# Optimization experiments

Hardware: AMD Instinct MI355X
Metric: run time of the kernel (lower is better)

## Reference

```python
import jax, jax.numpy as jnp
import numpy as np

B, S, I, H = 8, 2048, 8, 256
HEADS, HD = 4, 64
DECAY = 0.95


def _lstm_layer(x, w_ih, w_hh, b_ih, b_hh):
    # x: [B, S, in]; torch gate order i, f, g, o
    Hs = w_hh.shape[1]
    x_proj = jnp.einsum('bsi,gi->bsg', x, w_ih) + b_ih + b_hh  # [B,S,4H]
    def step(carry, xt):
        h, c = carry
        gates = xt + h @ w_hh.T
        i, f, g, o = jnp.split(gates, 4, axis=-1)
        c = jax.nn.sigmoid(f) * c + jax.nn.sigmoid(i) * jnp.tanh(g)
        h = jax.nn.sigmoid(o) * jnp.tanh(c)
        return (h, c), h
    h0 = jnp.zeros((x.shape[0], Hs), x.dtype)
    (_, _), hs = jax.lax.scan(step, (h0, h0), jnp.swapaxes(x_proj, 0, 1))
    return jnp.swapaxes(hs, 0, 1)  # [B,S,H]


def setup_inputs() -> dict:
    key = jax.random.key(0)
    ks = jax.random.split(key, 25)
    sc = lambda n: 1.0 / np.sqrt(n)
    d = {}
    d['x'] = jax.random.normal(ks[0], (B, S, I), jnp.float32)
    # LSTM layer 0 (in=I) and layer 1 (in=H)
    d['w_ih0'] = jax.random.uniform(ks[1], (4 * H, I), jnp.float32, -sc(H), sc(H))
    d['w_hh0'] = jax.random.uniform(ks[2], (4 * H, H), jnp.float32, -sc(H), sc(H))
    d['b_ih0'] = jax.random.uniform(ks[3], (4 * H,), jnp.float32, -sc(H), sc(H))
    d['b_hh0'] = jax.random.uniform(ks[4], (4 * H,), jnp.float32, -sc(H), sc(H))
    d['w_ih1'] = jax.random.uniform(ks[5], (4 * H, H), jnp.float32, -sc(H), sc(H))
    d['w_hh1'] = jax.random.uniform(ks[6], (4 * H, H), jnp.float32, -sc(H), sc(H))
    d['b_ih1'] = jax.random.uniform(ks[7], (4 * H,), jnp.float32, -sc(H), sc(H))
    d['b_hh1'] = jax.random.uniform(ks[8], (4 * H,), jnp.float32, -sc(H), sc(H))
    # attention projections [H,H] (+bias)
    for i, n in enumerate(['q', 'k', 'v', 'o']):
        d['w' + n] = jax.random.normal(ks[9 + 2 * i], (H, H), jnp.float32) * sc(H)
        d['b' + n] = jnp.zeros((H,), jnp.float32)
    # dual heads [5,H]
    d['w_mean'] = jax.random.normal(ks[20], (5, H), jnp.float32) * sc(H)
    d['b_mean'] = jnp.zeros((5,), jnp.float32)
    d['w_var'] = jax.random.normal(ks[21], (5, H), jnp.float32) * sc(H)
    d['b_var'] = jnp.zeros((5,), jnp.float32)
    return d


def reference(x, w_ih0, w_hh0, b_ih0, b_hh0, w_ih1, w_hh1, b_ih1, b_hh1,
              wq, bq, wk, bk, wv, bv, wo, bo, w_mean, b_mean, w_var, b_var):
    # 2-layer LSTM (dropout between layers is identity in eval)
    h = _lstm_layer(x, w_ih0, w_hh0, b_ih0, b_hh0)
    h = _lstm_layer(h, w_ih1, w_hh1, b_ih1, b_hh1)  # [B,S,H]
    # temporal decay attention
    idx = jnp.arange(S)
    decay = DECAY ** jnp.abs(idx[None, :] - idx[:, None]).astype(jnp.float32)  # [S,S]
    def proj(w, b):
        return (h @ w.T + b).reshape(B, S, HEADS, HD).transpose(0, 2, 1, 3)
    q, k, v = proj(wq, bq), proj(wk, bk), proj(wv, bv)  # [B,He,S,HD]
    scores = jnp.einsum('bhqd,bhkd->bhqk', q, k) / np.sqrt(HD)
    scores = scores * decay  # multiplicative decay mask
    probs = jax.nn.softmax(scores, axis=-1)
    attn = jnp.einsum('bhqk,bhkd->bhqd', probs, v)
    attn = attn.transpose(0, 2, 1, 3).reshape(B, S, H)
    attn = attn @ wo.T + bo
    context = attn[:, -1, :]  # last token; dropout identity in eval
    mean = context @ w_mean.T + b_mean
    log_var = context @ w_var.T + b_var
    return (mean, log_var)
```

## Files before the change

### kernel.cpp

```cpp
#include <hip/hip_runtime.h>
#include <math.h>

#define BATCH 8
#define SEQ   2048
#define IN    8
#define HID   256
#define G4    1024
#define XPR_R 64

typedef unsigned long long u64;
typedef unsigned int u32;


__device__ __forceinline__ float sigmoidf_(float x) { return 1.0f / (1.0f + __expf(-x)); }
__device__ __forceinline__ float tanhf_(float x) { return 1.0f - 2.0f / (__expf(2.0f * x) + 1.0f); }
__device__ __forceinline__ int hpad(int k) { return k + 4 * (k >> 5); }

__device__ __forceinline__ void light_barrier() {
    __asm__ volatile("s_waitcnt lgkmcnt(0)\n\ts_barrier" ::: "memory");
}

__device__ __forceinline__ float dpp_add8(float v) {
    int x;
    x = __builtin_amdgcn_update_dpp(0, __float_as_int(v), 0xB1, 0xF, 0xF, false);
    v += __int_as_float(x);
    x = __builtin_amdgcn_update_dpp(0, __float_as_int(v), 0x4E, 0xF, 0xF, false);
    v += __int_as_float(x);
    x = __builtin_amdgcn_update_dpp(0, __float_as_int(v), 0x141, 0xF, 0xF, false);
    v += __int_as_float(x);
    return v;
}

__device__ __forceinline__ float poll_tag(const u64* p, u32 tag) {
    u64 v;
    do { v = __hip_atomic_load(p, __ATOMIC_RELAXED, __HIP_MEMORY_SCOPE_AGENT); }
    while ((u32)(v >> 32) != tag);
    return __uint_as_float((u32)v);
}
__device__ __forceinline__ void pub_tag(u64* p, u32 tag, float x) {
    __hip_atomic_store(p, ((u64)tag << 32) | (u64)__float_as_uint(x),
                       __ATOMIC_RELAXED, __HIP_MEMORY_SCOPE_AGENT);
}

__device__ __forceinline__ void pin_f4(float4& v) {
    __asm__ volatile("" : "+v"(v.x), "+v"(v.y), "+v"(v.z), "+v"(v.w));
}

__device__ __forceinline__ void matvec8(const float4 (&w4)[4][8], const float* hrow, int ks,
                                        float& a0, float& a1, float& a2, float& a3) {
    a0 = a1 = a2 = a3 = 0.0f;
#pragma unroll
    for (int i = 0; i < 8; i++) {
        const float4 h4 = *(const float4*)(&hrow[36 * ks + 4 * i]);
        a0 += w4[0][i].x*h4.x + w4[0][i].y*h4.y + w4[0][i].z*h4.z + w4[0][i].w*h4.w;
        a1 += w4[1][i].x*h4.x + w4[1][i].y*h4.y + w4[1][i].z*h4.z + w4[1][i].w*h4.w;
        a2 += w4[2][i].x*h4.x + w4[2][i].y*h4.y + w4[2][i].z*h4.z + w4[2][i].w*h4.w;
        a3 += w4[3][i].x*h4.x + w4[3][i].y*h4.y + w4[3][i].z*h4.z + w4[3][i].w*h4.w;
    }
}

__global__
__attribute__((amdgpu_flat_work_group_size(512, 512)))
__attribute__((amdgpu_waves_per_eu(2, 2)))
void lstm_fused(
    const float* __restrict__ x,
    const float* __restrict__ w_ih0, const float* __restrict__ w_hh0,
    const float* __restrict__ b_ih0, const float* __restrict__ b_hh0,
    const float* __restrict__ w_ih1, const float* __restrict__ w_hh1,
    const float* __restrict__ b_ih1, const float* __restrict__ b_hh1,
    u64* __restrict__ h0s,
    u64* __restrict__ xpr,
    u64* __restrict__ h1r,
    float* __restrict__ hbuf)
{
    const int bid = blockIdx.x;
    const int b    = bid & 7;
    const int role = bid >> 3;
    const int grp  = role >> 2;
    const int q    = role & 3;
    const int t    = threadIdx.x;
    const int ks   = t & 7;
    const int rg   = t >> 3;
    const int wv   = t >> 6;
    const int lane = t & 63;
    const bool isg = (ks == 0);

    __shared__ float h_lds[2][288];
    __shared__ float xbuf[2][256];

    u64* h0b = h0s + (size_t)b * SEQ * HID;
    u64* xpb = xpr + (size_t)b * XPR_R * G4;

    for (int i = t; i < 576; i += 512) ((float*)h_lds)[i] = 0.0f;
    __syncthreads();

    if (grp == 0) {
        float4 w4[4][8];
#pragma unroll
        for (int j = 0; j < 4; j++) {
            const float4* wr = (const float4*)(w_hh0 + (size_t)(256*j + 64*q + rg) * HID + ks * 32);
#pragma unroll
            for (int i = 0; i < 8; i++) { w4[j][i] = wr[i]; pin_f4(w4[j][i]); }
        }
        float4 wi[4][2]; float bs4[4];
#pragma unroll
        for (int j = 0; j < 4; j++) {
            const int G = 256*j + 64*q + rg;
            wi[j][0] = *(const float4*)(w_ih0 + (size_t)G * IN);
            wi[j][1] = *(const float4*)(w_ih0 + (size_t)G * IN + 4);
            bs4[j] = b_ih0[G] + b_hh0[G];
        }
        const float* xb = x + (size_t)b * SEQ * IN;
        float c = 0.0f;
        float xv0 = 0, xv1 = 0, xv2 = 0, xv3 = 0;
        if (isg) {
            const float4 xa = *(const float4*)(xb);
            const float4 xc = *(const float4*)(xb + 4);
            xv0 = bs4[0] + wi[0][0].x*xa.x + wi[0][0].y*xa.y + wi[0][0].z*xa.z + wi[0][0].w*xa.w
                         + wi[0][1].x*xc.x + wi[0][1].y*xc.y + wi[0][1].z*xc.z + wi[0][1].w*xc.w;
            xv1 = bs4[1] + wi[1][0].x*xa.x + wi[1][0].y*xa.y + wi[1][0].z*xa.z + wi[1][0].w*xa.w
                         + wi[1][1].x*xc.x + wi[1][1].y*xc.y + wi[1][1].z*xc.z + wi[1][1].w*xc.w;
            xv2 = bs4[2] + wi[2][0].x*xa.x + wi[2][0].y*xa.y + wi[2][0].z*xa.z + wi[2][0].w*xa.w
                         + wi[2][1].x*xc.x + wi[2][1].y*xc.y + wi[2][1].z*xc.z + wi[2][1].w*xc.w;
            xv3 = bs4[3] + wi[3][0].x*xa.x + wi[3][0].y*xa.y + wi[3][0].z*xa.z + wi[3][0].w*xa.w
                         + wi[3][1].x*xc.x + wi[3][1].y*xc.y + wi[3][1].z*xc.z + wi[3][1].w*xc.w;
        }

        for (int s = 0; s < SEQ; s++) {
            const int cur = s & 1, nxt = cur ^ 1;
            float xn0 = 0, xn1 = 0, xn2 = 0, xn3 = 0;
            if (isg && s + 1 < SEQ) {
                const float4 xa = *(const float4*)(xb + (size_t)(s + 1) * IN);
                const float4 xc = *(const float4*)(xb + (size_t)(s + 1) * IN + 4);
                xn0 = bs4[0] + wi[0][0].x*xa.x + wi[0][0].y*xa.y + wi[0][0].z*xa.z + wi[0][0].w*xa.w
                             + wi[0][1].x*xc.x + wi[0][1].y*xc.y + wi[0][1].z*xc.z + wi[0][1].w*xc.w;
                xn1 = bs4[1] + wi[1][0].x*xa.x + wi[1][0].y*xa.y + wi[1][0].z*xa.z + wi[1][0].w*xa.w
                             + wi[1][1].x*xc.x + wi[1][1].y*xc.y + wi[1][1].z*xc.z + wi[1][1].w*xc.w;
                xn2 = bs4[2] + wi[2][0].x*xa.x + wi[2][0].y*xa.y + wi[2][0].z*xa.z + wi[2][0].w*xa.w
                             + wi[2][1].x*xc.x + wi[2][1].y*xc.y + wi[2][1].z*xc.z + wi[2][1].w*xc.w;
                xn3 = bs4[3] + wi[3][0].x*xa.x + wi[3][0].y*xa.y + wi[3][0].z*xa.z + wi[3][0].w*xa.w
                             + wi[3][1].x*xc.x + wi[3][1].y*xc.y + wi[3][1].z*xc.z + wi[3][1].w*xc.w;
            }
            float a0, a1, a2, a3;
            matvec8(w4, h_lds[cur], ks, a0, a1, a2, a3);
            a0 = dpp_add8(a0); a1 = dpp_add8(a1); a2 = dpp_add8(a2); a3 = dpp_add8(a3);
            const u32 tag = (u32)(s + 1);
            if (isg) {
                const float iv = sigmoidf_(a0 + xv0);
                const float fv = sigmoidf_(a1 + xv1);
                const float gv = tanhf_(a2 + xv2);
                const float ov = sigmoidf_(a3 + xv3);
                c = fv * c + iv * gv;
                const float hv = ov * tanhf_(c);
                const int u = 64*q + rg;
                pub_tag(&h0b[(size_t)s * HID + u], tag, hv);
                h_lds[nxt][hpad(u)] = hv;
                xv0 = xn0; xv1 = xn1; xv2 = xn2; xv3 = xn3;
            }
            if (wv >= 1 && wv <= 3) {
                const int u = 64 * ((q + wv) & 3) + lane;
                h_lds[nxt][hpad(u)] = poll_tag(&h0b[(size_t)s * HID + u], tag);
            }
            light_barrier();
        }
    } else if (grp == 1) {
        const int p = q;
        float4 w4[4][8]; float bs4[4];
#pragma unroll
        for (int j = 0; j < 4; j++) {
            const int R = 256*p + 64*j + rg;
            const float4* wr = (const float4*)(w_ih1 + (size_t)R * HID + ks * 32);
#pragma unroll
            for (int i = 0; i < 8; i++) { w4[j][i] = wr[i]; pin_f4(w4[j][i]); }
            bs4[j] = b_ih1[R] + b_hh1[R];
        }
        if (wv >= 4) {
            const int u = 64 * (wv - 4) + lane;
            h_lds[0][hpad(u)] = poll_tag(&h0b[u], 1u);
        }
        __syncthreads();

        for (int s = 0; s < SEQ; s++) {
            const int cur = s & 1, nxt = cur ^ 1;
            float a0, a1, a2, a3;
            matvec8(w4, h_lds[cur], ks, a0, a1, a2, a3);
            a0 = dpp_add8(a0); a1 = dpp_add8(a1); a2 = dpp_add8(a2); a3 = dpp_add8(a3);
            const u32 tag = (u32)(s + 1);
            if (isg) {
                if (s >= XPR_R) {
                    const u32 need = (u32)(s - (XPR_R - 1));
                    const u64* bp = h1r + ((size_t)(need & 1u) * 8 + b) * HID + (64*p + rg);
                    u32 tt;
                    do { tt = (u32)(__hip_atomic_load(bp, __ATOMIC_RELAXED, __HIP_MEMORY_SCOPE_AGENT) >> 32); }
                    while (!(tt >= need && tt <= 2048u));
                }
                u64* slot = xpb + (size_t)(s & (XPR_R - 1)) * G4 + 256*p + rg;
                pub_tag(slot +   0, tag, a0 + bs4[0]);
                pub_tag(slot +  64, tag, a1 + bs4[1]);
                pub_tag(slot + 128, tag, a2 + bs4[2]);
                pub_tag(slot + 192, tag, a3 + bs4[3]);
            }
            if (wv >= 4 && s + 1 < SEQ) {
                const int u = 64 * (wv - 4) + lane;
                h_lds[nxt][hpad(u)] = poll_tag(&h0b[(size_t)(s + 1) * HID + u], tag + 1u);
            }
            light_barrier();
        }
    } else {
        float4 w4[4][8];
#pragma unroll
        for (int j = 0; j < 4; j++) {
            const float4* wr = (const float4*)(w_hh1 + (size_t)(256*j + 64*q + rg) * HID + ks * 32);
#pragma unroll
            for (int i = 0; i < 8; i++) { w4[j][i] = wr[i]; pin_f4(w4[j][i]); }
        }
        float* ho = hbuf + (size_t)b * SEQ * HID;
        if (wv >= 4) {
            const int j = wv - 4;
            xbuf[0][64*j + lane] = poll_tag(&xpb[256*j + 64*q + lane], 1u);
        }
        __syncthreads();

        float c = 0.0f;
        for (int s = 0; s < SEQ; s++) {
            const int cur = s & 1, nxt = cur ^ 1;
            float a0, a1, a2, a3;
            matvec8(w4, h_lds[cur], ks, a0, a1, a2, a3);
            a0 = dpp_add8(a0); a1 = dpp_add8(a1); a2 = dpp_add8(a2); a3 = dpp_add8(a3);
            const u32 tag = (u32)(s + 1);
            if (isg) {
                const float xq0 = xbuf[cur][rg];
                const float xq1 = xbuf[cur][64 + rg];
                const float xq2 = xbuf[cur][128 + rg];
                const float xq3 = xbuf[cur][192 + rg];
                const float iv = sigmoidf_(a0 + xq0);
                const float fv = sigmoidf_(a1 + xq1);
                const float gv = tanhf_(a2 + xq2);
                const float ov = sigmoidf_(a3 + xq3);
                c = fv * c + iv * gv;
                const float hv = ov * tanhf_(c);
                const int u = 64*q + rg;
                pub_tag(&h1r[((size_t)(tag & 1u) * 8 + b) * HID + u], tag, hv);
                h_lds[nxt][hpad(u)] = hv;
                ho[(size_t)s * HID + u] = hv;
            }
            if (wv >= 1 && wv <= 3) {
                const int u = 64 * ((q + wv) & 3) + lane;
                h_lds[nxt][hpad(u)] = poll_tag(&h1r[((size_t)(tag & 1u) * 8 + b) * HID + u], tag);
            }
            if (wv >= 4 && s + 1 < SEQ) {
                const int j = wv - 4;
                xbuf[nxt][64*j + lane] =
                    poll_tag(&xpb[(size_t)((s + 1) & (XPR_R - 1)) * G4 + 256*j + 64*q + lane], tag + 1u);
            }
            light_barrier();
        }
    }
}

__global__ __launch_bounds__(256) void gemm_kv(
    const float* __restrict__ A,
    const float* __restrict__ Wk, const float* __restrict__ bk,
    const float* __restrict__ Wv, const float* __restrict__ bv,
    float* __restrict__ Ck, float* __restrict__ Cv, int M, int N, int K)
{
    const float* W    = blockIdx.z ? Wv : Wk;
    const float* bias = blockIdx.z ? bv : bk;
    float*       C    = blockIdx.z ? Cv : Ck;

    __shared__ float As[16][132];
    __shared__ float Bs[16][132];
    const int tid = threadIdx.x;
    const int tx = tid & 15;
    const int ty = tid >> 4;
    const int bm = blockIdx.x * 128;
    const int bn = blockIdx.y * 128;
    const int lrow = tid >> 1;
    const int lk = (tid & 1) * 8;

    float acc[8][8] = {};

    for (int k0 = 0; k0 < K; k0 += 16) {
        const float* ap = A + (size_t)(bm + lrow) * K + k0 + lk;
        const float* wp = W + (size_t)(bn + lrow) * K + k0 + lk;
        const float4 a0 = *(const float4*)ap;
        const float4 a1 = *(const float4*)(ap + 4);
        const float4 w0 = *(const float4*)wp;
        const float4 w1 = *(const float4*)(wp + 4);
        __syncthreads();
        As[lk+0][lrow] = a0.x; As[lk+1][lrow] = a0.y; As[lk+2][lrow] = a0.z; As[lk+3][lrow] = a0.w;
        As[lk+4][lrow] = a1.x; As[lk+5][lrow] = a1.y; As[lk+6][lrow] = a1.z; As[lk+7][lrow] = a1.w;
        Bs[lk+0][lrow] = w0.x; Bs[lk+1][lrow] = w0.y; Bs[lk+2][lrow] = w0.z; Bs[lk+3][lrow] = w0.w;
        Bs[lk+4][lrow] = w1.x; Bs[lk+5][lrow] = w1.y; Bs[lk+6][lrow] = w1.z; Bs[lk+7][lrow] = w1.w;
        __syncthreads();
#pragma unroll
        for (int k = 0; k < 16; k++) {
            const float4 av0 = *(const float4*)(&As[k][ty * 4]);
            const float4 av1 = *(const float4*)(&As[k][64 + ty * 4]);
            const float4 bv0 = *(const float4*)(&Bs[k][tx * 4]);
            const float4 bv1 = *(const float4*)(&Bs[k][64 + tx * 4]);
            const float ar[8] = {av0.x, av0.y, av0.z, av0.w, av1.x, av1.y, av1.z, av1.w};
            const float br[8] = {bv0.x, bv0.y, bv0.z, bv0.w, bv1.x, bv1.y, bv1.z, bv1.w};
#pragma unroll
            for (int i = 0; i < 8; i++)
#pragma unroll
                for (int j = 0; j < 8; j++) acc[i][j] += ar[i] * br[j];
        }
    }

    const int c0 = bn + tx * 4, c1 = bn + 64 + tx * 4;
    const float4 bb0 = *(const float4*)(bias + c0);
    const float4 bb1 = *(const float4*)(bias + c1);
#pragma unroll
    for (int ih = 0; ih < 2; ih++)
#pragma unroll
        for (int i = 0; i < 4; i++) {
            const int row = bm + ih * 64 + ty * 4 + i;
            const int ai = ih * 4 + i;
            float4 o0, o1;
            o0.x = acc[ai][0] + bb0.x; o0.y = acc[ai][1] + bb0.y;
            o0.z = acc[ai][2] + bb0.z; o0.w = acc[ai][3] + bb0.w;
            o1.x = acc[ai][4] + bb1.x; o1.y = acc[ai][5] + bb1.y;
            o1.z = acc[ai][6] + bb1.z; o1.w = acc[ai][7] + bb1.w;
            *(float4*)(C + (size_t)row * N + c0) = o0;
            *(float4*)(C + (size_t)row * N + c1) = o1;
        }
}

__global__ __launch_bounds__(256) void qlast_kernel(
    const float* __restrict__ h1, const float* __restrict__ wq,
    const float* __restrict__ bq, float* __restrict__ qout)
{
    const int b = blockIdx.x;
    const int t = threadIdx.x;
    __shared__ __align__(16) float hs[HID];
    hs[t] = h1[((size_t)b * SEQ + (SEQ - 1)) * HID + t];
    __syncthreads();
    const float4* wr = (const float4*)(wq + (size_t)t * HID);
    float acc = 0.0f;
#pragma unroll
    for (int k = 0; k < 64; k++) {
        const float4 wv = wr[k];
        const float4 hv = ((const float4*)hs)[k];
        acc += wv.x*hv.x + wv.y*hv.y + wv.z*hv.z + wv.w*hv.w;
    }
    qout[b * HID + t] = acc + bq[t];
}

__global__ __launch_bounds__(256) void attn_kernel(
    const float* __restrict__ Kb, const float* __restrict__ Vb,
    const float* __restrict__ q, float* __restrict__ attn)
{
    const int b = blockIdx.x >> 2;
    const int h = blockIdx.x & 3;
    const int tid = threadIdx.x;

    __shared__ __align__(16) float qs[64];
    __shared__ float sc[SEQ];
    __shared__ float red[256];
    __shared__ float part[4][64];

    if (tid < 64) qs[tid] = q[b * HID + h * 64 + tid];
    __syncthreads();

    const float LN095 = -0.051293294387550533f;
    for (int k = tid; k < SEQ; k += 256) {
        const float4* kr = (const float4*)(Kb + ((size_t)b * SEQ + k) * HID + h * 64);
        float acc = 0.0f;
#pragma unroll
        for (int d = 0; d < 16; d++) {
            const float4 kv = kr[d];
            const float4 qv = ((const float4*)qs)[d];
            acc += kv.x*qv.x + kv.y*qv.y + kv.z*qv.z + kv.w*qv.w;
        }
        const float dec = __expf(LN095 * (float)(SEQ - 1 - k));
        sc[k] = acc * 0.125f * dec;
    }
    __syncthreads();

    float m = -INFINITY;
    for (int k = tid; k < SEQ; k += 256) m = fmaxf(m, sc[k]);
    red[tid] = m;
    for (int off = 128; off > 0; off >>= 1) {
        __syncthreads();
        if (tid < off) red[tid] = fmaxf(red[tid], red[tid + off]);
    }
    __syncthreads();
    const float mx = red[0];

    float local = 0.0f;
    for (int k = tid; k < SEQ; k += 256) {
        const float p = expf(sc[k] - mx);
        sc[k] = p;
        local += p;
    }
    __syncthreads();
    red[tid] = local;
    for (int off = 128; off > 0; off >>= 1) {
        __syncthreads();
        if (tid < off) red[tid] += red[tid + off];
    }
    __syncthreads();
    const float total = red[0];

    const int chunk = tid >> 6;
    const int d = tid & 63;
    float acc = 0.0f;
    const int k0 = chunk * (SEQ / 4), k1 = (chunk + 1) * (SEQ / 4);
    for (int k = k0; k < k1; k++)
        acc += sc[k] * Vb[((size_t)b * SEQ + k) * HID + h * 64 + d];
    part[chunk][d] = acc;
    __syncthreads();
    if (tid < 64) {
        const float r = (part[0][tid] + part[1][tid]) + (part[2][tid] + part[3][tid]);
        attn[b * HID + h * 64 + tid] = r / total;
    }
}

__global__ __launch_bounds__(256) void head_kernel(
    const float* __restrict__ attn, const float* __restrict__ wo,
    const float* __restrict__ bo, const float* __restrict__ w_mean,
    const float* __restrict__ b_mean, const float* __restrict__ w_var,
    const float* __restrict__ b_var, float* __restrict__ out)
{
    const int b = blockIdx.x;
    const int t = threadIdx.x;
    __shared__ __align__(16) float av[HID];
    __shared__ __align__(16) float ctx[HID];
    av[t] = attn[b * HID + t];
    __syncthreads();
    {
        const float4* wr = (const float4*)(wo + (size_t)t * HID);
        float acc = 0.0f;
#pragma unroll
        for (int k = 0; k < 64; k++) {
            const float4 wv = wr[k];
            const float4 hv = ((const float4*)av)[k];
            acc += wv.x*hv.x + wv.y*hv.y + wv.z*hv.z + wv.w*hv.w;
        }
        ctx[t] = acc + bo[t];
    }
    __syncthreads();
    if (t < 5) {
        const float4* wr = (const float4*)(w_mean + (size_t)t * HID);
        float acc = 0.0f;
#pragma unroll
        for (int k = 0; k < 64; k++) {
            const float4 wv = wr[k];
            const float4 hv = ((const float4*)ctx)[k];
            acc += wv.x*hv.x + wv.y*hv.y + wv.z*hv.z + wv.w*hv.w;
        }
        out[b * 5 + t] = acc + b_mean[t];
    } else if (t >= 8 && t < 13) {
        const int m = t - 8;
        const float4* wr = (const float4*)(w_var + (size_t)m * HID);
        float acc = 0.0f;
#pragma unroll
        for (int k = 0; k < 64; k++) {
            const float4 wv = wr[k];
            const float4 hv = ((const float4*)ctx)[k];
            acc += wv.x*hv.x + wv.y*hv.y + wv.z*hv.z + wv.w*hv.w;
        }
        out[BATCH * 5 + b * 5 + m] = acc + b_var[m];
    }
}

extern "C" void kernel_launch(void* const* d_in, const int* in_sizes, int n_in,
                              void* d_out, int out_size, void* d_ws, size_t ws_size,
                              hipStream_t stream) {
    const float* x      = (const float*)d_in[0];
    const float* w_ih0  = (const float*)d_in[1];
    const float* w_hh0  = (const float*)d_in[2];
    const float* b_ih0  = (const float*)d_in[3];
    const float* b_hh0  = (const float*)d_in[4];
    const float* w_ih1  = (const float*)d_in[5];
    const float* w_hh1  = (const float*)d_in[6];
    const float* b_ih1  = (const float*)d_in[7];
    const float* b_hh1  = (const float*)d_in[8];
    const float* wq     = (const float*)d_in[9];
    const float* bq     = (const float*)d_in[10];
    const float* wk     = (const float*)d_in[11];
    const float* bk     = (const float*)d_in[12];
    const float* wvv    = (const float*)d_in[13];
    const float* bv     = (const float*)d_in[14];
    const float* wo     = (const float*)d_in[15];
    const float* bo     = (const float*)d_in[16];
    const float* w_mean = (const float*)d_in[17];
    const float* b_mean = (const float*)d_in[18];
    const float* w_var  = (const float*)d_in[19];
    const float* b_var  = (const float*)d_in[20];
    float* out = (float*)d_out;

    char* wsb = (char*)d_ws;
    u64*  h0s  = (u64*)(wsb);
    u64*  xpr  = (u64*)(wsb + 33554432);
    u64*  h1r  = (u64*)(wsb + 37748736);
    float* hbuf = (float*)(wsb + 37781504);
    float* Kbuf = (float*)(wsb);
    float* Vbuf = (float*)(wsb + 16777216);
    float* qbuf = (float*)(wsb + 33554432);
    float* abuf = (float*)(wsb + 33554432 + 8192);

    lstm_fused<<<96, 512, 0, stream>>>(x, w_ih0, w_hh0, b_ih0, b_hh0,
                                       w_ih1, w_hh1, b_ih1, b_hh1,
                                       h0s, xpr, h1r, hbuf);
    gemm_kv<<<dim3(128, 2, 2), 256, 0, stream>>>(hbuf, wk, bk, wvv, bv, Kbuf, Vbuf, 16384, 256, 256);
    qlast_kernel<<<BATCH, 256, 0, stream>>>(hbuf, wq, bq, qbuf);
    attn_kernel<<<BATCH * 4, 256, 0, stream>>>(Kbuf, Vbuf, qbuf, abuf);
    head_kernel<<<BATCH, 256, 0, stream>>>(abuf, wo, bo, w_mean, b_mean, w_var, b_var, out);
}
```

Before: 3.673 ms.

## Use packed fp16 weights and hidden state with v_dot2 in LSTM matvecs

Converts the register-resident recurrent and input weights to packed fp16 pairs and stores the hidden state in LDS as packed fp16 pairs. The per-step matvec then uses v_dot2_f32_f16, halving the multiply instructions, LDS reads and weight registers. Neighbouring h values are combined with DPP shuffles before each packed LDS write. The intent is to shorten the serial per-step critical path, at the cost of fp16 rounding in the recurrence, which can accumulate error over 2048 steps.

```diff
diff --git a/kernel.cpp b/kernel.cpp
--- a/kernel.cpp
+++ b/kernel.cpp
@@ -10,11 +10,19 @@
 
 typedef unsigned long long u64;
 typedef unsigned int u32;
+typedef _Float16 f16;
 
 
 __device__ __forceinline__ float sigmoidf_(float x) { return 1.0f / (1.0f + __expf(-x)); }
 __device__ __forceinline__ float tanhf_(float x) { return 1.0f - 2.0f / (__expf(2.0f * x) + 1.0f); }
-__device__ __forceinline__ int hpad(int k) { return k + 4 * (k >> 5); }
+
+__device__ __forceinline__ int hword(int p) { return p + 4 * (p >> 4); }
+
+__device__ __forceinline__ u32 pk2h(float a, float b) {
+    unsigned short ua = __builtin_bit_cast(unsigned short, (f16)a);
+    unsigned short ub = __builtin_bit_cast(unsigned short, (f16)b);
+    return (u32)ua | ((u32)ub << 16);
+}
 
 __device__ __forceinline__ void light_barrier() {
     __asm__ volatile("s_waitcnt lgkmcnt(0)\n\ts_barrier" ::: "memory");
@@ -42,21 +50,44 @@
                        __ATOMIC_RELAXED, __HIP_MEMORY_SCOPE_AGENT);
 }
 
-__device__ __forceinline__ void pin_f4(float4& v) {
-    __asm__ volatile("" : "+v"(v.x), "+v"(v.y), "+v"(v.z), "+v"(v.w));
-}
-
-__device__ __forceinline__ void matvec8(const float4 (&w4)[4][8], const float* hrow, int ks,
-                                        float& a0, float& a1, float& a2, float& a3) {
+__device__ __forceinline__ void pin1(u32& v) { __asm__ volatile("" : "+v"(v)); }
+
+#define DOT2(ACC, W, H) __asm__("v_dot2_f32_f16 %0, %1, %2, %0" : "+v"(ACC) : "v"(W), "v"(H))
+
+__device__ __forceinline__ void matvec8p(const u32 (&wp)[4][16], const u32* hl, int ks,
+                                         float& a0, float& a1, float& a2, float& a3) {
     a0 = a1 = a2 = a3 = 0.0f;
 #pragma unroll
-    for (int i = 0; i < 8; i++) {
-        const float4 h4 = *(const float4*)(&hrow[36 * ks + 4 * i]);
-        a0 += w4[0][i].x*h4.x + w4[0][i].y*h4.y + w4[0][i].z*h4.z + w4[0][i].w*h4.w;
-        a1 += w4[1][i].x*h4.x + w4[1][i].y*h4.y + w4[1][i].z*h4.z + w4[1][i].w*h4.w;
-        a2 += w4[2][i].x*h4.x + w4[2][i].y*h4.y + w4[2][i].z*h4.z + w4[2][i].w*h4.w;
-        a3 += w4[3][i].x*h4.x + w4[3][i].y*h4.y + w4[3][i].z*h4.z + w4[3][i].w*h4.w;
-    }
+    for (int i = 0; i < 4; i++) {
+        const uint4 h4 = *(const uint4*)(hl + 20 * ks + 4 * i);
+        DOT2(a0, wp[0][4*i+0], h4.x); DOT2(a0, wp[0][4*i+1], h4.y);
+        DOT2(a0, wp[0][4*i+2], h4.z); DOT2(a0, wp[0][4*i+3], h4.w);
+        DOT2(a1, wp[1][4*i+0], h4.x); DOT2(a1, wp[1][4*i+1], h4.y);
+        DOT2(a1, wp[1][4*i+2], h4.z); DOT2(a1, wp[1][4*i+3], h4.w);
+        DOT2(a2, wp[2][4*i+0], h4.x); DOT2(a2, wp[2][4*i+1], h4.y);
+        DOT2(a2, wp[2][4*i+2], h4.z); DOT2(a2, wp[2][4*i+3], h4.w);
+        DOT2(a3, wp[3][4*i+0], h4.x); DOT2(a3, wp[3][4*i+1], h4.y);
+        DOT2(a3, wp[3][4*i+2], h4.z); DOT2(a3, wp[3][4*i+3], h4.w);
+    }
+}
+
+__device__ __forceinline__ void load_w_packed(const float* __restrict__ W, int r0, int r1,
+                                              int r2, int r3, int colbase, u32 (&wp)[4][16]) {
+    const int rows[4] = {r0, r1, r2, r3};
+#pragma unroll
+    for (int j = 0; j < 4; j++) {
+        const float4* wr = (const float4*)(W + (size_t)rows[j] * HID + colbase);
+#pragma unroll
+        for (int i = 0; i < 8; i++) {
+            const float4 f = wr[i];
+            wp[j][2*i]   = pk2h(f.x, f.y);
+            wp[j][2*i+1] = pk2h(f.z, f.w);
+        }
+    }
+#pragma unroll
+    for (int j = 0; j < 4; j++)
+#pragma unroll
+        for (int k = 0; k < 16; k++) pin1(wp[j][k]);
 }
 
 __global__
@@ -85,23 +116,19 @@
     const int lane = t & 63;
     const bool isg = (ks == 0);
 
-    __shared__ float h_lds[2][288];
+    __shared__ __align__(16) u32 h_pk[2][160];
     __shared__ float xbuf[2][256];
 
     u64* h0b = h0s + (size_t)b * SEQ * HID;
     u64* xpb = xpr + (size_t)b * XPR_R * G4;
 
-    for (int i = t; i < 576; i += 512) ((float*)h_lds)[i] = 0.0f;
+    for (int i = t; i < 320; i += 512) ((u32*)h_pk)[i] = 0u;
     __syncthreads();
 
     if (grp == 0) {
-        float4 w4[4][8];
-#pragma unroll
-        for (int j = 0; j < 4; j++) {
-            const float4* wr = (const float4*)(w_hh0 + (size_t)(256*j + 64*q + rg) * HID + ks * 32);
-#pragma unroll
-            for (int i = 0; i < 8; i++) { w4[j][i] = wr[i]; pin_f4(w4[j][i]); }
-        }
+        u32 wp[4][16];
+        load_w_packed(w_hh0, 64*q + rg, 256 + 64*q + rg, 512 + 64*q + rg, 768 + 64*q + rg,
+                      ks * 32, wp);
         float4 wi[4][2]; float bs4[4];
 #pragma unroll
         for (int j = 0; j < 4; j++) {
@@ -142,7 +169,7 @@
                              + wi[3][1].x*xc.x + wi[3][1].y*xc.y + wi[3][1].z*xc.z + wi[3][1].w*xc.w;
             }
             float a0, a1, a2, a3;
-            matvec8(w4, h_lds[cur], ks, a0, a1, a2, a3);
+            matvec8p(wp, h_pk[cur], ks, a0, a1, a2, a3);
             a0 = dpp_add8(a0); a1 = dpp_add8(a1); a2 = dpp_add8(a2); a3 = dpp_add8(a3);
             const u32 tag = (u32)(s + 1);
             if (isg) {
@@ -154,36 +181,43 @@
                 const float hv = ov * tanhf_(c);
                 const int u = 64*q + rg;
                 pub_tag(&h0b[(size_t)s * HID + u], tag, hv);
-                h_lds[nxt][hpad(u)] = hv;
+                const int nb = __builtin_amdgcn_update_dpp(0, __float_as_int(hv), 0x108, 0xF, 0xF, false);
+                if ((rg & 1) == 0)
+                    h_pk[nxt][hword(32*q + (rg >> 1))] = pk2h(hv, __int_as_float(nb));
                 xv0 = xn0; xv1 = xn1; xv2 = xn2; xv3 = xn3;
             }
             if (wv >= 1 && wv <= 3) {
                 const int u = 64 * ((q + wv) & 3) + lane;
-                h_lds[nxt][hpad(u)] = poll_tag(&h0b[(size_t)s * HID + u], tag);
+                const float pv = poll_tag(&h0b[(size_t)s * HID + u], tag);
+                const int nb = __builtin_amdgcn_update_dpp(0, __float_as_int(pv), 0xB1, 0xF, 0xF, false);
+                if ((lane & 1) == 0)
+                    h_pk[nxt][hword(32*((q + wv) & 3) + (lane >> 1))] = pk2h(pv, __int_as_float(nb));
             }
             light_barrier();
         }
     } else if (grp == 1) {
         const int p = q;
-        float4 w4[4][8]; float bs4[4];
+        u32 wp[4][16]; float bs4[4];
+        load_w_packed(w_ih1, 256*p + rg, 256*p + 64 + rg, 256*p + 128 + rg, 256*p + 192 + rg,
+                      ks * 32, wp);
 #pragma unroll
         for (int j = 0; j < 4; j++) {
             const int R = 256*p + 64*j + rg;
-            const float4* wr = (const float4*)(w_ih1 + (size_t)R * HID + ks * 32);
-#pragma unroll
-            for (int i = 0; i < 8; i++) { w4[j][i] = wr[i]; pin_f4(w4[j][i]); }
             bs4[j] = b_ih1[R] + b_hh1[R];
         }
         if (wv >= 4) {
             const int u = 64 * (wv - 4) + lane;
-            h_lds[0][hpad(u)] = poll_tag(&h0b[u], 1u);
+            const float pv = poll_tag(&h0b[u], 1u);
+            const int nb = __builtin_amdgcn_update_dpp(0, __float_as_int(pv), 0xB1, 0xF, 0xF, false);
+            if ((lane & 1) == 0)
+                h_pk[0][hword(32*(wv - 4) + (lane >> 1))] = pk2h(pv, __int_as_float(nb));
         }
         __syncthreads();
 
         for (int s = 0; s < SEQ; s++) {
             const int cur = s & 1, nxt = cur ^ 1;
             float a0, a1, a2, a3;
-            matvec8(w4, h_lds[cur], ks, a0, a1, a2, a3);
+            matvec8p(wp, h_pk[cur], ks, a0, a1, a2, a3);
             a0 = dpp_add8(a0); a1 = dpp_add8(a1); a2 = dpp_add8(a2); a3 = dpp_add8(a3);
             const u32 tag = (u32)(s + 1);
             if (isg) {
@@ -202,18 +236,17 @@
             }
             if (wv >= 4 && s + 1 < SEQ) {
                 const int u = 64 * (wv - 4) + lane;
-                h_lds[nxt][hpad(u)] = poll_tag(&h0b[(size_t)(s + 1) * HID + u], tag + 1u);
+                const float pv = poll_tag(&h0b[(size_t)(s + 1) * HID + u], tag + 1u);
+                const int nb = __builtin_amdgcn_update_dpp(0, __float_as_int(pv), 0xB1, 0xF, 0xF, false);
+                if ((lane & 1) == 0)
+                    h_pk[nxt][hword(32*(wv - 4) + (lane >> 1))] = pk2h(pv, __int_as_float(nb));
             }
             light_barrier();
         }
     } else {
-        float4 w4[4][8];
-#pragma unroll
-        for (int j = 0; j < 4; j++) {
-            const float4* wr = (const float4*)(w_hh1 + (size_t)(256*j + 64*q + rg) * HID + ks * 32);
-#pragma unroll
-            for (int i = 0; i < 8; i++) { w4[j][i] = wr[i]; pin_f4(w4[j][i]); }
-        }
+        u32 wp[4][16];
+        load_w_packed(w_hh1, 64*q + rg, 256 + 64*q + rg, 512 + 64*q + rg, 768 + 64*q + rg,
+                      ks * 32, wp);
         float* ho = hbuf + (size_t)b * SEQ * HID;
         if (wv >= 4) {
             const int j = wv - 4;
@@ -225,7 +258,7 @@
         for (int s = 0; s < SEQ; s++) {
             const int cur = s & 1, nxt = cur ^ 1;
             float a0, a1, a2, a3;
-            matvec8(w4, h_lds[cur], ks, a0, a1, a2, a3);
+            matvec8p(wp, h_pk[cur], ks, a0, a1, a2, a3);
             a0 = dpp_add8(a0); a1 = dpp_add8(a1); a2 = dpp_add8(a2); a3 = dpp_add8(a3);
             const u32 tag = (u32)(s + 1);
             if (isg) {
@@ -241,12 +274,17 @@
                 const float hv = ov * tanhf_(c);
                 const int u = 64*q + rg;
                 pub_tag(&h1r[((size_t)(tag & 1u) * 8 + b) * HID + u], tag, hv);
-                h_lds[nxt][hpad(u)] = hv;
+                const int nb = __builtin_amdgcn_update_dpp(0, __float_as_int(hv), 0x108, 0xF, 0xF, false);
+                if ((rg & 1) == 0)
+                    h_pk[nxt][hword(32*q + (rg >> 1))] = pk2h(hv, __int_as_float(nb));
                 ho[(size_t)s * HID + u] = hv;
             }
             if (wv >= 1 && wv <= 3) {
                 const int u = 64 * ((q + wv) & 3) + lane;
-                h_lds[nxt][hpad(u)] = poll_tag(&h1r[((size_t)(tag & 1u) * 8 + b) * HID + u], tag);
+                const float pv = poll_tag(&h1r[((size_t)(tag & 1u) * 8 + b) * HID + u], tag);
+                const int nb = __builtin_amdgcn_update_dpp(0, __float_as_int(pv), 0xB1, 0xF, 0xF, false);
+                if ((lane & 1) == 0)
+                    h_pk[nxt][hword(32*((q + wv) & 3) + (lane >> 1))] = pk2h(pv, __int_as_float(nb));
             }
             if (wv >= 4 && s + 1 < SEQ) {
                 const int j = wv - 4;
```

After: 3.528 ms. 3.9% less time.
